# Performance work log

Hardware: AMD Instinct MI355X
Metric: run time of the kernel (lower is better)

The kernel has to match this reference:

```python
import math
import jax, jax.numpy as jnp
import numpy as np

EMBED_DIM = 1024
NUM_HEADS = 16
HEAD_DIM = EMBED_DIM // NUM_HEADS
B, S = 4, 2048


def setup_inputs() -> dict:
    key = jax.random.key(0)
    ks = jax.random.split(key, 12)
    sc = 1.0 / math.sqrt(EMBED_DIM)
    inp = {
        "query": jax.random.normal(ks[0], (B, S, EMBED_DIM), jnp.float32),
        "key": jax.random.normal(ks[1], (B, S, EMBED_DIM), jnp.float32),
        "value": jax.random.normal(ks[2], (B, S, EMBED_DIM), jnp.float32),
        # causal mask: True = masked (upper triangle above diagonal)
        "attn_mask": jnp.triu(jnp.ones((S, S), jnp.bool_), k=1),
        "q_w": jax.random.normal(ks[3], (EMBED_DIM, EMBED_DIM), jnp.float32) * sc,
        "q_b": jax.random.normal(ks[4], (EMBED_DIM,), jnp.float32) * sc,
        "k_w": jax.random.normal(ks[5], (EMBED_DIM, EMBED_DIM), jnp.float32) * sc,
        "k_b": jax.random.normal(ks[6], (EMBED_DIM,), jnp.float32) * sc,
        "v_w": jax.random.normal(ks[7], (EMBED_DIM, EMBED_DIM), jnp.float32) * sc,
        "v_b": jax.random.normal(ks[8], (EMBED_DIM,), jnp.float32) * sc,
        "o_w": jax.random.normal(ks[9], (EMBED_DIM, EMBED_DIM), jnp.float32) * sc,
        "o_b": jax.random.normal(ks[10], (EMBED_DIM,), jnp.float32) * sc,
    }
    return inp


def _split_heads(x):
    # (B, S, E) -> (B, H, S, D)
    b, s, _ = x.shape
    return x.reshape(b, s, NUM_HEADS, HEAD_DIM).transpose(0, 2, 1, 3)


def reference(query, key, value, attn_mask, q_w, q_b, k_w, k_b, v_w, v_b, o_w, o_b):
    # torch Linear: y = x @ W.T + b
    q = _split_heads(query @ q_w.T + q_b)
    k = _split_heads(key @ k_w.T + k_b)
    v = _split_heads(value @ v_w.T + v_b)
    scale = math.sqrt(HEAD_DIM)
    scores = jnp.einsum("bhqd,bhkd->bhqk", q, k) / scale
    scores = jnp.where(attn_mask[None, None, :, :], -jnp.inf, scores)
    attn = jax.nn.softmax(scores, axis=-1)
    ctx = jnp.einsum("bhqk,bhkd->bhqd", attn, v)  # (B,H,S,D)
    ctx = ctx.transpose(0, 2, 1, 3).reshape(query.shape[0], query.shape[1], EMBED_DIM)
    return ctx @ o_w.T + o_b
```

## Files before the change

### kernel.cpp

```cpp
#include <hip/hip_runtime.h>
#include <stdint.h>

#define BB 4
#define SS 2048
#define EE 1024
#define HH 16
#define DD 64
#define MM (BB*SS)

typedef unsigned short u16;
typedef __attribute__((ext_vector_type(8))) short bf16x8;
typedef __attribute__((ext_vector_type(4))) float f32x4;

#define MFMA __builtin_amdgcn_mfma_f32_16x16x32_bf16

#if __has_builtin(__builtin_amdgcn_exp2f)
#define EXP2(x) __builtin_amdgcn_exp2f(x)
#else
#define EXP2(x) exp2f(x)
#endif

__device__ __forceinline__ u16 f2bf(float f) {
  union { float f; uint32_t u; } x; x.f = f;
  uint32_t r = (x.u + 0x7fffu + ((x.u >> 16) & 1u)) >> 16;
  return (u16)r;
}

__device__ __forceinline__ uint32_t cvtpk(float lo, float hi) {
  uint32_t r;
  asm volatile("v_cvt_pk_bf16_f32 %0, %1, %2" : "=v"(r) : "v"(lo), "v"(hi));
  return r;
}

__device__ __forceinline__ void gl_lds16(const void* g, void* l) {
  __builtin_amdgcn_global_load_lds(
      (const __attribute__((address_space(1))) uint32_t*)g,
      (__attribute__((address_space(3))) uint32_t*)l, 16, 0, 0);
}

__global__ __launch_bounds__(256) void cast_w(
    const float* __restrict__ s0, const float* __restrict__ s1,
    const float* __restrict__ s2, const float* __restrict__ s3,
    u16* __restrict__ d0, u16* __restrict__ d1,
    u16* __restrict__ d2, u16* __restrict__ d3) {
  int i = blockIdx.x * 256 + threadIdx.x;
  int sel = i >> 17, off = i & ((1 << 17) - 1);
  const float* s = sel == 0 ? s0 : sel == 1 ? s1 : sel == 2 ? s2 : s3;
  u16* d = sel == 0 ? d0 : sel == 1 ? d1 : sel == 2 ? d2 : d3;
  const float4* sp = (const float4*)s;
  float4 a = sp[off*2], b = sp[off*2+1];
  union { u16 h[8]; uint4 v; } o;
  o.h[0]=f2bf(a.x); o.h[1]=f2bf(a.y); o.h[2]=f2bf(a.z); o.h[3]=f2bf(a.w);
  o.h[4]=f2bf(b.x); o.h[5]=f2bf(b.y); o.h[6]=f2bf(b.z); o.h[7]=f2bf(b.w);
  *(uint4*)(d + (size_t)off*8) = o.v;
}

template<int A_FP32, int OUT_BF16>
__device__ __forceinline__ void gemm_body(
    const void* __restrict__ Ap, const u16* __restrict__ W,
    const float* __restrict__ bias, void* __restrict__ Cout,
    int Ndim, int Kdim, float scale, int m0, int n0,
    u16* As, u16* Bs) {
  const int tid = threadIdx.x;
  const int lane = tid & 63, w = tid >> 6;
  const int wr = w >> 1, wc = w & 1;
  const int l15 = lane & 15;
  const int l4 = lane >> 4;
  const int fke = l4 * 8;

  f32x4 acc[4][4] = {};

  const int srow = tid >> 2;
  const int scol = (tid & 3) * 8;
  const u16* bg = W + (size_t)(n0 + srow) * Kdim + scol;
  const size_t rstrideB = (size_t)64 * Kdim;

  const int ar  = tid >> 3;
  const int asl = tid & 7;
  const int asw = asl ^ (ar & 7);
  const float* agf = nullptr;
  const u16*   agh = nullptr;
  if (A_FP32) agf = (const float*)Ap + (size_t)(m0 + ar) * Kdim + asw * 4;
  else        agh = (const u16*)Ap + (size_t)(m0 + srow) * Kdim + scol;

  char* AsB = (char*)As;

  for (int k0 = 0; k0 < Kdim; k0 += 32) {
    if (A_FP32) {
      #pragma unroll
      for (int i = 0; i < 4; ++i)
        gl_lds16(agf + (size_t)i*32*Kdim + k0, AsB + i*4096 + tid*16);
    } else {
      gl_lds16(agh + k0,                     As + tid*8);
      gl_lds16(agh + k0 + (size_t)64*Kdim,   As + 2048 + tid*8);
    }
    gl_lds16(bg + k0,            Bs + tid*8);
    gl_lds16(bg + k0 + rstrideB, Bs + 2048 + tid*8);
    __syncthreads();

    bf16x8 af[4], bfr[4];
    #pragma unroll
    for (int m = 0; m < 4; ++m) {
      int r = wr*64 + m*16 + l15;
      if (A_FP32) {
        const char* rb = AsB + r*128;
        f32x4 fa = *(const f32x4*)(rb + (((l4*2    ) ^ (r & 7)) * 16));
        f32x4 fb = *(const f32x4*)(rb + (((l4*2 + 1) ^ (r & 7)) * 16));
        union { uint32_t u[4]; bf16x8 v; } cv;
        cv.u[0] = cvtpk(fa[0], fa[1]);
        cv.u[1] = cvtpk(fa[2], fa[3]);
        cv.u[2] = cvtpk(fb[0], fb[1]);
        cv.u[3] = cvtpk(fb[2], fb[3]);
        af[m] = cv.v;
      } else {
        af[m] = *(const bf16x8*)(As + r*32 + fke);
      }
    }
    #pragma unroll
    for (int n = 0; n < 4; ++n)
      bfr[n] = *(const bf16x8*)(Bs + (wc*64 + n*16 + l15)*32 + fke);
    #pragma unroll
    for (int m = 0; m < 4; ++m)
      #pragma unroll
      for (int n = 0; n < 4; ++n)
        acc[m][n] = MFMA(af[m], bfr[n], acc[m][n], 0, 0, 0);
    __syncthreads();
  }

  const int ccol = wc*64 + l15;
  float bv[4];
  #pragma unroll
  for (int n = 0; n < 4; ++n) bv[n] = bias[n0 + ccol + n*16];
  #pragma unroll
  for (int m = 0; m < 4; ++m) {
    #pragma unroll
    for (int i = 0; i < 4; ++i) {
      size_t row = (size_t)(m0 + wr*64 + m*16 + l4*4 + i);
      #pragma unroll
      for (int n = 0; n < 4; ++n) {
        float v = (acc[m][n][i] + bv[n]) * scale;
        size_t idx = row * Ndim + (n0 + ccol + n*16);
        if (OUT_BF16) ((u16*)Cout)[idx] = f2bf(v);
        else          ((float*)Cout)[idx] = v;
      }
    }
  }
}

__global__ __launch_bounds__(256, 2) void gemm_qkv(
    const float* __restrict__ qx, const float* __restrict__ kx, const float* __restrict__ vx,
    const u16* __restrict__ wqm, const u16* __restrict__ wkm, const u16* __restrict__ wvm,
    const float* __restrict__ qbv, const float* __restrict__ kbv, const float* __restrict__ vbv,
    u16* __restrict__ qo, u16* __restrict__ ko, u16* __restrict__ vo) {
  __shared__ alignas(16) u16 As[128*64];
  __shared__ alignas(16) u16 Bs[128*32];
  const int flat = blockIdx.x + blockIdx.y * 8 + blockIdx.z * 512;
  const int j = flat & 7, s = flat >> 3;
  const int c = 6*j + (s >> 5), i = s & 31;
  const int nx = i & 7;
  const int my = ((c & 15) << 2) + (i >> 3);
  const int z = c >> 4;
  const float* A = z == 0 ? qx : z == 1 ? kx : vx;
  const u16* W = z == 0 ? wqm : z == 1 ? wkm : wvm;
  const float* bias = z == 0 ? qbv : z == 1 ? kbv : vbv;
  u16* C = z == 0 ? qo : z == 1 ? ko : vo;
  const float scale = z == 0 ? 0.125f : 1.0f;
  gemm_body<1,1>(A, W, bias, C, EE, EE, scale, my * 128, nx * 128, As, Bs);
}

__global__ __launch_bounds__(256, 2) void gemm_out(
    const u16* __restrict__ A, const u16* __restrict__ W,
    const float* __restrict__ bias, float* __restrict__ Cout) {
  __shared__ alignas(16) u16 As[128*32];
  __shared__ alignas(16) u16 Bs[128*32];
  const int flat = blockIdx.x + blockIdx.y * 8;
  const int j = flat & 7, s = flat >> 3;
  const int nx = s & 7, yy = (j << 3) + (s >> 3);
  gemm_body<0,0>(A, W, bias, Cout, EE, EE, 1.0f, yy * 128, nx * 128, As, Bs);
}

__global__ __launch_bounds__(256, 2) void attn9(
    const u16* __restrict__ Q, const u16* __restrict__ K,
    const u16* __restrict__ V, u16* __restrict__ ctx) {
  __shared__ alignas(16) u16 Ks[2][2][64*64];
  __shared__ alignas(16) u16 VTs[2][2][64*64];
  __shared__ alignas(16) u16 Ps[4][32*64];

  const int tid = threadIdx.x, lane = tid & 63, w = tid >> 6;
  const int l15 = lane & 15, l4 = lane >> 4;

  const int f = blockIdx.x;
  const int j = f & 7, s = f >> 3;
  const int qlo = s & 7;
  const int panel = j * 8 + (s >> 3);
  const int h = panel & 15, b = panel >> 4;
  const size_t base = ((size_t)b * SS) * EE + h * DD;

  const int kr  = tid >> 3;
  const int ksl = tid & 7;
  const int rv  = tid >> 2;
  const int vc  = tid & 3;

  u16* KsE  = (u16*)Ks;
  u16* VTsE = (u16*)VTs;
  u16* PsE  = (u16*)Ps + w * 2048;

  auto stageK = [&](int t, int pb, int sub) {
    #pragma unroll
    for (int i = 0; i < 2; ++i) {
      int row = i*32 + kr;
      gl_lds16(K + base + (size_t)(t*64 + row)*EE + (ksl ^ (row & 7))*8,
               KsE + pb*8192 + sub*4096 + i*2048 + tid*8);
    }
  };
  auto vtWrite = [&](int pb, int sub, bf16x8 v0, bf16x8 v1) {
    #pragma unroll
    for (int jj = 0; jj < 16; ++jj) {
      u16 val = jj < 8 ? (u16)v0[jj] : (u16)v1[jj - 8];
      int d = vc*16 + jj;
      int sl = (rv >> 3) ^ (jj & 7) ^ (vc << 1);
      VTsE[pb*8192 + sub*4096 + d*64 + sl*8 + (rv & 7)] = val;
    }
  };

  #pragma unroll 1
  for (int pass = 0; pass < 2; ++pass) {
    const int qblk = pass == 0 ? (15 - qlo) : qlo;
    const int q0 = qblk * 128, wq = q0 + w * 32;
    const int npairs = qblk + 1;

    bf16x8 qf[2][2];
    #pragma unroll
    for (int G = 0; G < 2; ++G)
      #pragma unroll
      for (int kc = 0; kc < 2; ++kc)
        qf[G][kc] = *(const bf16x8*)(Q + base + (size_t)(wq + G*16 + l15)*EE + kc*32 + l4*8);

    f32x4 o[2][4] = {};
    float lsum[2] = {0.f, 0.f};

    auto computeTile = [&](int t, int pb, int sub) {
      if (wq + 31 < t*64) return;
      const bool g0act = (wq + 15 >= t*64);
      const u16* tileK = KsE + pb*8192 + sub*4096;
      const u16* tileV = VTsE + pb*8192 + sub*4096;

      f32x4 sc[2][4] = {};
      #pragma unroll
      for (int nt = 0; nt < 4; ++nt) {
        int row = nt*16 + l15;
        int sw = row & 7;
        const u16* kb = tileK + row*64;
        bf16x8 kf0 = *(const bf16x8*)(kb + ((l4    ) ^ sw)*8);
        bf16x8 kf1 = *(const bf16x8*)(kb + ((4 + l4) ^ sw)*8);
        sc[1][nt] = MFMA(kf0, qf[1][0], sc[1][nt], 0, 0, 0);
        sc[1][nt] = MFMA(kf1, qf[1][1], sc[1][nt], 0, 0, 0);
        if (g0act) {
          sc[0][nt] = MFMA(kf0, qf[0][0], sc[0][nt], 0, 0, 0);
          sc[0][nt] = MFMA(kf1, qf[0][1], sc[0][nt], 0, 0, 0);
        }
      }

      #pragma unroll
      for (int G = 0; G < 2; ++G) {
        if (G == 0 && !g0act) continue;
        const bool nomask = (t*64 + 63 <= wq + G*16);
        const int qg = wq + G*16 + l15;
        #pragma unroll
        for (int nt = 0; nt < 4; ++nt) {
          float p0 = EXP2(__builtin_fmaf(sc[G][nt][0], 1.44269504f, -17.3123405f));
          float p1 = EXP2(__builtin_fmaf(sc[G][nt][1], 1.44269504f, -17.3123405f));
          float p2 = EXP2(__builtin_fmaf(sc[G][nt][2], 1.44269504f, -17.3123405f));
          float p3 = EXP2(__builtin_fmaf(sc[G][nt][3], 1.44269504f, -17.3123405f));
          if (!nomask) {
            int kvs = t*64 + nt*16 + l4*4;
            if (kvs + 0 > qg) p0 = 0.f;
            if (kvs + 1 > qg) p1 = 0.f;
            if (kvs + 2 > qg) p2 = 0.f;
            if (kvs + 3 > qg) p3 = 0.f;
          }
          lsum[G] += (p0 + p1) + (p2 + p3);
          uint2 pk;
          pk.x = cvtpk(p0, p1);
          pk.y = cvtpk(p2, p3);
          *(uint2*)((char*)PsE + (G*16 + l15)*128
                        + (((nt*2 + (l4 >> 1)) ^ (l15 & 7)) * 16)
                        + (l4 & 1) * 8) = pk;
        }
      }

      #pragma unroll
      for (int cc = 0; cc < 2; ++cc) {
        bf16x8 pf1 = *(const bf16x8*)((char*)PsE + (16 + l15)*128
                                     + (((cc*4 + l4) ^ (l15 & 7)) * 16));
        bf16x8 pf0;
        if (g0act)
          pf0 = *(const bf16x8*)((char*)PsE + l15*128
                                     + (((cc*4 + l4) ^ (l15 & 7)) * 16));
        #pragma unroll
        for (int dm = 0; dm < 4; ++dm) {
          int sl = (cc*4 + l4) ^ (l15 & 7) ^ (dm << 1);
          bf16x8 vfv = *(const bf16x8*)(tileV + (dm*16 + l15)*64 + sl*8);
          o[1][dm] = MFMA(pf1, vfv, o[1][dm], 0, 0, 0);
          if (g0act) o[0][dm] = MFMA(pf0, vfv, o[0][dm], 0, 0, 0);
        }
      }
    };

    {
      const u16* va = V + base + (size_t)rv*EE + vc*16;
      const u16* vb = V + base + (size_t)(64 + rv)*EE + vc*16;
      bf16x8 a0 = *(const bf16x8*)va, a1 = *(const bf16x8*)(va + 8);
      bf16x8 b0 = *(const bf16x8*)vb, b1 = *(const bf16x8*)(vb + 8);
      stageK(0, 0, 0);
      stageK(1, 0, 1);
      vtWrite(0, 0, a0, a1);
      vtWrite(0, 1, b0, b1);
    }
    __syncthreads();

    for (int u = 0; u < npairs; ++u) {
      const int cur = u & 1;
      const bool havenext = (u + 1 < npairs);
      bf16x8 na0, na1, nb0, nb1;
      if (havenext) {
        const u16* va = V + base + (size_t)((2*u+2)*64 + rv)*EE + vc*16;
        const u16* vb = V + base + (size_t)((2*u+3)*64 + rv)*EE + vc*16;
        na0 = *(const bf16x8*)va; na1 = *(const bf16x8*)(va + 8);
        nb0 = *(const bf16x8*)vb; nb1 = *(const bf16x8*)(vb + 8);
        stageK(2*u+2, cur ^ 1, 0);
        stageK(2*u+3, cur ^ 1, 1);
      }

      computeTile(2*u, cur, 0);
      if (havenext) vtWrite(cur ^ 1, 0, na0, na1);
      computeTile(2*u + 1, cur, 1);
      if (havenext) vtWrite(cur ^ 1, 1, nb0, nb1);
      __syncthreads();
    }

    #pragma unroll
    for (int G = 0; G < 2; ++G) {
      float r = lsum[G];
      r += __shfl_xor(r, 16);
      r += __shfl_xor(r, 32);
      lsum[G] = 1.0f / r;
    }

    #pragma unroll
    for (int G = 0; G < 2; ++G)
      #pragma unroll
      for (int i = 0; i < 4; ++i) {
        float invv = __shfl(lsum[G], l4*4 + i);
        size_t roff = base + (size_t)(wq + G*16 + l4*4 + i) * EE;
        #pragma unroll
        for (int dm = 0; dm < 4; ++dm)
          ctx[roff + dm*16 + l15] = f2bf(o[G][dm][i] * invv);
      }
  }
}

extern "C" void kernel_launch(void* const* d_in, const int* in_sizes, int n_in,
                              void* d_out, int out_size, void* d_ws, size_t ws_size,
                              hipStream_t stream) {
  const float* query = (const float*)d_in[0];
  const float* key   = (const float*)d_in[1];
  const float* value = (const float*)d_in[2];
  const float* q_w = (const float*)d_in[4];
  const float* q_b = (const float*)d_in[5];
  const float* k_w = (const float*)d_in[6];
  const float* k_b = (const float*)d_in[7];
  const float* v_w = (const float*)d_in[8];
  const float* v_b = (const float*)d_in[9];
  const float* o_w = (const float*)d_in[10];
  const float* o_b = (const float*)d_in[11];

  char* ws = (char*)d_ws;
  const size_t XB = (size_t)MM * EE * 2;
  const size_t WB = (size_t)EE * EE * 2;
  u16* wq = (u16*)(ws);
  u16* wk = (u16*)(ws + WB);
  u16* wv = (u16*)(ws + 2*WB);
  u16* wo = (u16*)(ws + 3*WB);
  u16* qp = (u16*)(ws + 4*WB);
  u16* kp = (u16*)(ws + 4*WB + XB);
  u16* vp = (u16*)(ws + 4*WB + 2*XB);
  u16* ctxb = (u16*)(ws + 4*WB + 3*XB);

  const int nw8 = EE * EE / 8;
  cast_w<<<4*nw8/256, 256, 0, stream>>>(q_w, k_w, v_w, o_w, wq, wk, wv, wo);

  gemm_qkv<<<dim3(8, 64, 3), 256, 0, stream>>>(
      query, key, value, wq, wk, wv, q_b, k_b, v_b, qp, kp, vp);

  attn9<<<512, 256, 0, stream>>>(qp, kp, vp, ctxb);

  gemm_out<<<dim3(EE/128, MM/128), 256, 0, stream>>>(ctxb, wo, o_b, (float*)d_out);
}
```

Before: 175.6 us.

## Double-buffer GEMM LDS tiles, swizzle bf16 tiles, raise gemm_out occupancy

The shared GEMM body now double-buffers its LDS tiles. It issues the async global-to-LDS copy for the next K-step before computing the current one, so memory latency overlaps with MFMA work and only one barrier remains per iteration. The bf16 A/B tiles get an XOR swizzle on the 16-byte chunk index to cut LDS bank conflicts on fragment reads. gemm_out's launch bounds go from 2 to 4 blocks per CU. The cost is doubled LDS per block and more register pressure under the tighter occupancy bound.

```diff
diff --git a/kernel.cpp b/kernel.cpp
--- a/kernel.cpp
+++ b/kernel.cpp
@@ -60,50 +60,53 @@
     const void* __restrict__ Ap, const u16* __restrict__ W,
     const float* __restrict__ bias, void* __restrict__ Cout,
     int Ndim, int Kdim, float scale, int m0, int n0,
-    u16* As, u16* Bs) {
+    char* AsB, char* BsB) {
   const int tid = threadIdx.x;
   const int lane = tid & 63, w = tid >> 6;
   const int wr = w >> 1, wc = w & 1;
-  const int l15 = lane & 15;
-  const int l4 = lane >> 4;
-  const int fke = l4 * 8;
+  const int l15 = lane & 15, l4 = lane >> 4;
 
   f32x4 acc[4][4] = {};
 
-  const int srow = tid >> 2;
-  const int scol = (tid & 3) * 8;
-  const u16* bg = W + (size_t)(n0 + srow) * Kdim + scol;
+  const int srow = tid >> 2, st = tid & 3;
+  const int ssw = st ^ ((srow >> 1) & 3);
+  const u16* bg = W + (size_t)(n0 + srow) * Kdim + ssw * 8;
   const size_t rstrideB = (size_t)64 * Kdim;
 
-  const int ar  = tid >> 3;
-  const int asl = tid & 7;
+  const int ar = tid >> 3, asl = tid & 7;
   const int asw = asl ^ (ar & 7);
   const float* agf = nullptr;
   const u16*   agh = nullptr;
   if (A_FP32) agf = (const float*)Ap + (size_t)(m0 + ar) * Kdim + asw * 4;
-  else        agh = (const u16*)Ap + (size_t)(m0 + srow) * Kdim + scol;
-
-  char* AsB = (char*)As;
-
-  for (int k0 = 0; k0 < Kdim; k0 += 32) {
+  else        agh = (const u16*)Ap + (size_t)(m0 + srow) * Kdim + ssw * 8;
+
+  auto stage = [&](int k0, int bi) {
     if (A_FP32) {
       #pragma unroll
       for (int i = 0; i < 4; ++i)
-        gl_lds16(agf + (size_t)i*32*Kdim + k0, AsB + i*4096 + tid*16);
+        gl_lds16(agf + (size_t)i*32*Kdim + k0, AsB + bi*16384 + i*4096 + tid*16);
     } else {
-      gl_lds16(agh + k0,                     As + tid*8);
-      gl_lds16(agh + k0 + (size_t)64*Kdim,   As + 2048 + tid*8);
-    }
-    gl_lds16(bg + k0,            Bs + tid*8);
-    gl_lds16(bg + k0 + rstrideB, Bs + 2048 + tid*8);
-    __syncthreads();
+      gl_lds16(agh + k0,                    AsB + bi*8192 + tid*16);
+      gl_lds16(agh + k0 + (size_t)64*Kdim,  AsB + bi*8192 + 4096 + tid*16);
+    }
+    gl_lds16(bg + k0,            BsB + bi*8192 + tid*16);
+    gl_lds16(bg + k0 + rstrideB, BsB + bi*8192 + 4096 + tid*16);
+  };
+
+  stage(0, 0);
+  __syncthreads();
+
+  const int T = Kdim / 32;
+  for (int t = 0; t < T; ++t) {
+    const int bi = t & 1;
+    if (t + 1 < T) stage((t + 1) * 32, bi ^ 1);
 
     bf16x8 af[4], bfr[4];
     #pragma unroll
     for (int m = 0; m < 4; ++m) {
       int r = wr*64 + m*16 + l15;
       if (A_FP32) {
-        const char* rb = AsB + r*128;
+        const char* rb = AsB + bi*16384 + r*128;
         f32x4 fa = *(const f32x4*)(rb + (((l4*2    ) ^ (r & 7)) * 16));
         f32x4 fb = *(const f32x4*)(rb + (((l4*2 + 1) ^ (r & 7)) * 16));
         union { uint32_t u[4]; bf16x8 v; } cv;
@@ -113,12 +116,14 @@
         cv.u[3] = cvtpk(fb[2], fb[3]);
         af[m] = cv.v;
       } else {
-        af[m] = *(const bf16x8*)(As + r*32 + fke);
-      }
-    }
-    #pragma unroll
-    for (int n = 0; n < 4; ++n)
-      bfr[n] = *(const bf16x8*)(Bs + (wc*64 + n*16 + l15)*32 + fke);
+        af[m] = *(const bf16x8*)(AsB + bi*8192 + r*64 + ((l4 ^ ((r >> 1) & 3)) * 16));
+      }
+    }
+    #pragma unroll
+    for (int n = 0; n < 4; ++n) {
+      int rr = wc*64 + n*16 + l15;
+      bfr[n] = *(const bf16x8*)(BsB + bi*8192 + rr*64 + ((l4 ^ ((rr >> 1) & 3)) * 16));
+    }
     #pragma unroll
     for (int m = 0; m < 4; ++m)
       #pragma unroll
@@ -152,8 +157,8 @@
     const u16* __restrict__ wqm, const u16* __restrict__ wkm, const u16* __restrict__ wvm,
     const float* __restrict__ qbv, const float* __restrict__ kbv, const float* __restrict__ vbv,
     u16* __restrict__ qo, u16* __restrict__ ko, u16* __restrict__ vo) {
-  __shared__ alignas(16) u16 As[128*64];
-  __shared__ alignas(16) u16 Bs[128*32];
+  __shared__ alignas(16) char AsB[2*16384];
+  __shared__ alignas(16) char BsB[2*8192];
   const int flat = blockIdx.x + blockIdx.y * 8 + blockIdx.z * 512;
   const int j = flat & 7, s = flat >> 3;
   const int c = 6*j + (s >> 5), i = s & 31;
@@ -165,18 +170,18 @@
   const float* bias = z == 0 ? qbv : z == 1 ? kbv : vbv;
   u16* C = z == 0 ? qo : z == 1 ? ko : vo;
   const float scale = z == 0 ? 0.125f : 1.0f;
-  gemm_body<1,1>(A, W, bias, C, EE, EE, scale, my * 128, nx * 128, As, Bs);
-}
-
-__global__ __launch_bounds__(256, 2) void gemm_out(
+  gemm_body<1,1>(A, W, bias, C, EE, EE, scale, my * 128, nx * 128, AsB, BsB);
+}
+
+__global__ __launch_bounds__(256, 4) void gemm_out(
     const u16* __restrict__ A, const u16* __restrict__ W,
     const float* __restrict__ bias, float* __restrict__ Cout) {
-  __shared__ alignas(16) u16 As[128*32];
-  __shared__ alignas(16) u16 Bs[128*32];
+  __shared__ alignas(16) char AsB[2*8192];
+  __shared__ alignas(16) char BsB[2*8192];
   const int flat = blockIdx.x + blockIdx.y * 8;
   const int j = flat & 7, s = flat >> 3;
   const int nx = s & 7, yy = (j << 3) + (s >> 3);
-  gemm_body<0,0>(A, W, bias, Cout, EE, EE, 1.0f, yy * 128, nx * 128, As, Bs);
+  gemm_body<0,0>(A, W, bias, Cout, EE, EE, 1.0f, yy * 128, nx * 128, AsB, BsB);
 }
 
 __global__ __launch_bounds__(256, 2) void attn9(
```

Result: slower. 180.4 us (+2.7%).
